# Optimization experiments

Hardware: AMD Instinct MI355X
Metric: run time of the kernel (lower is better)

The kernel has to match this reference:

```python
import jax, jax.numpy as jnp
import numpy as np
import math

DIM = 1024
NUM_HEADS = 16
QUANTUM_HEADS = 2
HEAD_DIM = DIM // NUM_HEADS          # 64
TRAD_HEADS = NUM_HEADS - QUANTUM_HEADS  # 14
B, S = 1, 1024
STEPS = 2048
LN_EPS = 1e-5


def setup_inputs() -> dict:
    key = jax.random.key(0)
    ks = jax.random.split(key, 10)
    hd2 = 2 * HEAD_DIM
    return {
        "x": jax.random.normal(ks[0], (B, S, DIM), jnp.float32),
        # to_quantum_state: Linear(head_dim -> 2*head_dim) + LayerNorm + Tanh (shared across quantum heads)
        "qs_W": jax.random.normal(ks[1], (hd2, HEAD_DIM), jnp.float32) / math.sqrt(HEAD_DIM),
        "qs_b": jnp.zeros((hd2,), jnp.float32),
        "ln_g": jnp.ones((hd2,), jnp.float32),
        "ln_b": jnp.zeros((hd2,), jnp.float32),
        # per-quantum-head scalars
        "q_freq": jax.random.normal(ks[2], (QUANTUM_HEADS,), jnp.float32) * 0.02,
        "q_shift": jax.random.normal(ks[3], (QUANTUM_HEADS,), jnp.float32) * 0.02,
        # traditional head projections (no bias)
        "Wq": jax.random.normal(ks[4], (TRAD_HEADS * HEAD_DIM, DIM), jnp.float32) / math.sqrt(DIM),
        "Wk": jax.random.normal(ks[5], (TRAD_HEADS * HEAD_DIM, DIM), jnp.float32) / math.sqrt(DIM),
        "Wv": jax.random.normal(ks[6], (TRAD_HEADS * HEAD_DIM, DIM), jnp.float32) / math.sqrt(DIM),
        # output projection (with bias)
        "Wo": jax.random.normal(ks[7], (DIM, DIM), jnp.float32) / math.sqrt(DIM),
        "bo": jnp.zeros((DIM,), jnp.float32),
    }


def _layernorm(h, g, b):
    mu = jnp.mean(h, axis=-1, keepdims=True)
    var = jnp.mean(jnp.square(h - mu), axis=-1, keepdims=True)
    return (h - mu) * jax.lax.rsqrt(var + LN_EPS) * g + b


def _forward(x, qs_W, qs_b, ln_g, ln_b, q_freq, q_shift, Wq, Wk, Wv, Wo, bo):
    cos_table = jnp.cos(jnp.linspace(0.0, 2.0 * math.pi, STEPS).astype(jnp.float32))
    scale = 1.0 / math.sqrt(HEAD_DIM)
    two_pi = 2.0 * math.pi

    outs = []
    # ---- quantum heads (small fixed loop over structurally distinct heads) ----
    for h in range(QUANTUM_HEADS):
        xh = x[..., h * HEAD_DIM:(h + 1) * HEAD_DIM]          # (B,S,hd)
        qs = jnp.tanh(_layernorm(xh @ qs_W.T + qs_b, ln_g, ln_b))  # (B,S,2hd)
        amp, phase = jnp.split(qs, 2, axis=-1)                 # each (B,S,hd)
        # per (query pos i, key pos j, feature d) phase difference
        pd = (phase[:, :, None, :] - phase[:, None, :, :]) * q_freq[h] + q_shift[h]  # (B,S,S,hd)
        idx = jnp.floor(jnp.mod(pd / two_pi * STEPS, STEPS)).astype(jnp.int32)
        interf = cos_table[idx]                                # lookup-table gather, (B,S,S,hd)
        attn = jnp.einsum('bid,bjd,bijd->bij', amp, amp, interf) * scale
        attn = jax.nn.softmax(attn, axis=-1)
        outs.append(attn @ xh)                                 # (B,S,hd), values are the raw head slice

    # ---- traditional heads: standard multi-head attention ----
    q = (x @ Wq.T).reshape(B, S, TRAD_HEADS, HEAD_DIM)
    k = (x @ Wk.T).reshape(B, S, TRAD_HEADS, HEAD_DIM)
    v = (x @ Wv.T).reshape(B, S, TRAD_HEADS, HEAD_DIM)
    scores = jnp.einsum('bqhd,bkhd->bhqk', q, k) * scale       # (B,Ht,S,S)
    probs = jax.nn.softmax(scores, axis=-1)
    trad = jnp.einsum('bhqk,bkhd->bqhd', probs, v).reshape(B, S, TRAD_HEADS * HEAD_DIM)
    outs.append(trad)

    out = jnp.concatenate(outs, axis=-1)                       # (B,S,DIM)
    return out @ Wo.T + bo


def reference(x, qs_W, qs_b, ln_g, ln_b, q_freq, q_shift, Wq, Wk, Wv, Wo, bo):
    return _forward(x, qs_W, qs_b, ln_g, ln_b, q_freq, q_shift, Wq, Wk, Wv, Wo, bo)
```

## Files before the change

kernel.cpp:

```cpp
#include <hip/hip_runtime.h>
#include <hip/hip_bf16.h>
#include <math.h>

#define DIMX 1024
#define SEQ  1024
#define HD   64
#define QH   2
#define TH   14
#define QKVN 2688
#define LN_EPS 1e-5f
#define NB_F2B 4736
#define NB_QPREP 1024
#define NB_XT 32

typedef __bf16 bf16x8 __attribute__((ext_vector_type(8)));
typedef float  f32x4  __attribute__((ext_vector_type(4)));
typedef unsigned short u16x8 __attribute__((ext_vector_type(8)));

__device__ inline unsigned short f2b_rne(float f) {
  unsigned int u = __float_as_uint(f);
  unsigned int r = (u + 0x7FFF + ((u >> 16) & 1)) >> 16;
  return (unsigned short)r;
}

__device__ inline float waveRedSum(float v) {
  #pragma unroll
  for (int off = 32; off; off >>= 1) v += __shfl_xor(v, off, 64);
  return v;
}

__global__ __launch_bounds__(256) void k_prep(
    const float* __restrict__ x, const float* __restrict__ qsW,
    const float* __restrict__ qsb, const float* __restrict__ lng,
    const float* __restrict__ lnb, const float* __restrict__ qfreq,
    const float* __restrict__ qshift,
    const float* __restrict__ wq, const float* __restrict__ wk,
    const float* __restrict__ wv, const float* __restrict__ wo,
    unsigned short* __restrict__ x_bf, unsigned short* __restrict__ wqkv_bf,
    unsigned short* __restrict__ wo_bf,
    unsigned short* __restrict__ qcs, unsigned short* __restrict__ kcs,
    unsigned short* __restrict__ xt) {
  __shared__ float xrow2[2][HD];
  __shared__ float redm[2][2], redv[2][2];
  __shared__ float qsv2[2][128];
  __shared__ unsigned short ttile[64][72];
  int t = threadIdx.x;
  int bid = blockIdx.x;
  if (bid < NB_F2B) {
    long i = ((long)bid * 256 + t) * 4;
    float4 v;
    unsigned short* dst;
    if (i < 1048576) {
      v = *reinterpret_cast<const float4*>(x + i);
      dst = x_bf + i;
    } else if (i < 3801088) {
      long j = i - 1048576;
      const float* s = (j < 917504) ? wq + j
                     : (j < 1835008) ? wk + (j - 917504)
                                     : wv + (j - 1835008);
      v = *reinterpret_cast<const float4*>(s);
      dst = wqkv_bf + j;
    } else {
      long j = i - 3801088;
      v = *reinterpret_cast<const float4*>(wo + j);
      dst = wo_bf + j;
    }
    ushort4 o;
    o.x = f2b_rne(v.x); o.y = f2b_rne(v.y); o.z = f2b_rne(v.z); o.w = f2b_rne(v.w);
    *reinterpret_cast<ushort4*>(dst) = o;
  } else if (bid < NB_F2B + NB_QPREP) {
    int half = t >> 7, o = t & 127;
    int row = (bid - NB_F2B) * 2 + half;
    int h = row >> 10, i = row & 1023;
    if (o < HD) xrow2[half][o] = x[i * DIMX + h * HD + o];
    __syncthreads();
    float s = qsb[o];
    #pragma unroll
    for (int d = 0; d < HD; d += 4) {
      float4 w = *reinterpret_cast<const float4*>(qsW + o * HD + d);
      float4 xv = *reinterpret_cast<const float4*>(&xrow2[half][d]);
      s += xv.x * w.x + xv.y * w.y + xv.z * w.z + xv.w * w.w;
    }
    int wid = (o >> 6), lane = o & 63;
    float ws = waveRedSum(s);
    if (lane == 0) redm[half][wid] = ws;
    __syncthreads();
    float mu = (redm[half][0] + redm[half][1]) * (1.0f / 128.0f);
    float dv = s - mu;
    float ws2 = waveRedSum(dv * dv);
    if (lane == 0) redv[half][wid] = ws2;
    __syncthreads();
    float var = (redv[half][0] + redv[half][1]) * (1.0f / 128.0f);
    float y = dv * rsqrtf(var + LN_EPS) * lng[o] + lnb[o];
    qsv2[half][o] = tanhf(y);
    __syncthreads();
    float freq = qfreq[h], shift = qshift[h];
    size_t base = ((size_t)h * 1024 + i) * 128;
    if (o < HD) {
      float amp = qsv2[half][o];
      float a = qsv2[half][64 + o] * freq + shift;
      float sn, cs;
      __sincosf(a, &sn, &cs);
      qcs[base + o]      = f2b_rne(amp * cs);
      qcs[base + 64 + o] = f2b_rne(amp * sn);
    } else {
      int d = o - 64;
      float amp = qsv2[half][d];
      float bAng = qsv2[half][64 + d] * freq;
      float sn, cs;
      __sincosf(bAng, &sn, &cs);
      kcs[base + d]      = f2b_rne(amp * cs);
      kcs[base + 64 + d] = f2b_rne(amp * sn);
    }
  } else {
    int b = bid - (NB_F2B + NB_QPREP);
    int h = b >> 4, kv0 = (b & 15) * 64;
    #pragma unroll
    for (int pass = 0; pass < 2; ++pass) {
      int s = pass * 256 + t;
      int r = s >> 3, c8 = (s & 7) * 8;
      const float* src = x + (size_t)(kv0 + r) * DIMX + h * 64 + c8;
      float4 a = *reinterpret_cast<const float4*>(src);
      float4 b4 = *reinterpret_cast<const float4*>(src + 4);
      ushort4 o1, o2;
      o1.x = f2b_rne(a.x);  o1.y = f2b_rne(a.y);  o1.z = f2b_rne(a.z);  o1.w = f2b_rne(a.w);
      o2.x = f2b_rne(b4.x); o2.y = f2b_rne(b4.y); o2.z = f2b_rne(b4.z); o2.w = f2b_rne(b4.w);
      *reinterpret_cast<ushort4*>(&ttile[r][c8]) = o1;
      *reinterpret_cast<ushort4*>(&ttile[r][c8 + 4]) = o2;
    }
    __syncthreads();
    #pragma unroll
    for (int pass = 0; pass < 2; ++pass) {
      int s = pass * 256 + t;
      int d = s >> 3, k8 = (s & 7) * 8;
      u16x8 o;
      #pragma unroll
      for (int j = 0; j < 8; ++j) o[j] = ttile[k8 + j][d];
      *reinterpret_cast<u16x8*>(xt + (size_t)h * 65536 + (size_t)d * 1024 + kv0 + k8) = o;
    }
  }
}

template <int DQK, int NT>
__device__ __forceinline__ void dev_fattn2(
    char* smem,
    const unsigned short* __restrict__ Qp, int ldq,
    const unsigned short* __restrict__ Kp, int ldk,
    const unsigned short* __restrict__ Vp,
    int q0, int kv0, int slot,
    float* __restrict__ pout, float* __restrict__ pml) {
  const int LQ = DQK + 8;
  const int KREG = DQK / 32;
  unsigned short* KV0 = (unsigned short*)smem;
  unsigned short* KV1 = KV0 + 64 * LQ;
  unsigned short* Ps  = KV1 + 64 * LQ;
  int t = threadIdx.x, lane = t & 63, w = t >> 6;
  int g = lane >> 4, li = lane & 15;

  bf16x8 aq[KREG];
  #pragma unroll
  for (int kk = 0; kk < KREG; ++kk)
    aq[kk] = *reinterpret_cast<const bf16x8*>(
        Qp + (size_t)(q0 + w * 16 + li) * ldq + kk * 32 + g * 8);

  u16x8 kreg[KREG], vreg[2];
  auto loadK = [&](int tile) {
    int j0 = kv0 + tile * 64;
    #pragma unroll
    for (int i = 0; i < KREG; ++i) {
      int s = i * 256 + t;
      int r = s / (DQK / 8), c8 = (s % (DQK / 8)) * 8;
      kreg[i] = *reinterpret_cast<const u16x8*>(Kp + (size_t)(j0 + r) * ldk + c8);
    }
  };
  auto writeK = [&](int buf) {
    unsigned short* Kd = buf ? KV1 : KV0;
    #pragma unroll
    for (int i = 0; i < KREG; ++i) {
      int s = i * 256 + t;
      int r = s / (DQK / 8), c8 = (s % (DQK / 8)) * 8;
      *reinterpret_cast<u16x8*>(&Kd[r * LQ + c8]) = kreg[i];
    }
  };
  auto loadV = [&](int tile) {
    int j0 = kv0 + tile * 64;
    #pragma unroll
    for (int i = 0; i < 2; ++i) {
      int s = i * 256 + t;
      int d = s >> 3, c8 = (s & 7) * 8;
      vreg[i] = *reinterpret_cast<const u16x8*>(Vp + (size_t)d * 1024 + j0 + c8);
    }
  };
  auto writeV = [&](int buf) {
    unsigned short* Vd = buf ? KV1 : KV0;
    #pragma unroll
    for (int i = 0; i < 2; ++i) {
      int s = i * 256 + t;
      int d = s >> 3, c8 = (s & 7) * 8;
      *reinterpret_cast<u16x8*>(&Vd[d * 72 + c8]) = vreg[i];
    }
  };

  loadK(0); writeK(0);
  if (NT > 1) loadK(1);
  loadV(0);
  __syncthreads();

  f32x4 s_all[NT][4] = {};

  #pragma unroll
  for (int tile = 0; tile < NT; ++tile) {
    const unsigned short* Ksc = (tile & 1) ? KV1 : KV0;
    if (tile < NT - 1) writeK((tile + 1) & 1);
    if (tile < NT - 2) loadK(tile + 2);
    if (tile == NT - 1) writeV(0);
    #pragma unroll
    for (int kk = 0; kk < KREG; ++kk) {
      #pragma unroll
      for (int n = 0; n < 4; ++n) {
        bf16x8 bk = *reinterpret_cast<const bf16x8*>(&Ksc[(n * 16 + li) * LQ + kk * 32 + g * 8]);
        s_all[tile][n] = __builtin_amdgcn_mfma_f32_16x16x32_bf16(aq[kk], bk, s_all[tile][n], 0, 0, 0);
      }
    }
    __syncthreads();
  }

  if (NT > 1) loadV(1);

  float mrow[4], lrow[4];
  #pragma unroll
  for (int r = 0; r < 4; ++r) {
    float tm = -1e30f;
    #pragma unroll
    for (int tile = 0; tile < NT; ++tile)
      #pragma unroll
      for (int n = 0; n < 4; ++n) tm = fmaxf(tm, s_all[tile][n][r]);
    #pragma unroll
    for (int m = 1; m < 16; m <<= 1) tm = fmaxf(tm, __shfl_xor(tm, m, 64));
    float rs = 0.f;
    #pragma unroll
    for (int tile = 0; tile < NT; ++tile)
      #pragma unroll
      for (int n = 0; n < 4; ++n) {
        float p = __expf((s_all[tile][n][r] - tm) * 0.125f);
        s_all[tile][n][r] = p;
        rs += p;
      }
    #pragma unroll
    for (int m = 1; m < 16; m <<= 1) rs += __shfl_xor(rs, m, 64);
    mrow[r] = tm; lrow[r] = rs;
  }

  f32x4 acc_o[4] = {};
  #pragma unroll
  for (int tile = 0; tile < NT; ++tile) {
    const unsigned short* Vsc = (tile & 1) ? KV1 : KV0;
    if (tile < NT - 1) writeV((tile + 1) & 1);
    if (tile < NT - 2) loadV(tile + 2);
    #pragma unroll
    for (int n = 0; n < 4; ++n)
      #pragma unroll
      for (int r = 0; r < 4; ++r)
        Ps[(w * 16 + g * 4 + r) * 72 + n * 16 + li] = f2b_rne(s_all[tile][n][r]);
    #pragma unroll
    for (int kk = 0; kk < 2; ++kk) {
      bf16x8 ap = *reinterpret_cast<const bf16x8*>(&Ps[(w * 16 + li) * 72 + kk * 32 + g * 8]);
      #pragma unroll
      for (int n = 0; n < 4; ++n) {
        bf16x8 bv = *reinterpret_cast<const bf16x8*>(&Vsc[(n * 16 + li) * 72 + kk * 32 + g * 8]);
        acc_o[n] = __builtin_amdgcn_mfma_f32_16x16x32_bf16(ap, bv, acc_o[n], 0, 0, 0);
      }
    }
    __syncthreads();
  }

  size_t rowbase = (size_t)slot * 1024;
  #pragma unroll
  for (int r = 0; r < 4; ++r) {
    int qr = q0 + w * 16 + g * 4 + r;
    #pragma unroll
    for (int n = 0; n < 4; ++n)
      pout[(rowbase + qr) * 64 + n * 16 + li] = acc_o[n][r];
    if (li == 0) {
      pml[(rowbase + qr) * 2 + 0] = mrow[r];
      pml[(rowbase + qr) * 2 + 1] = lrow[r];
    }
  }
}

template <int HAS_BIAS, int BF16_OUT>
__device__ __forceinline__ void dev_gemm64(
    char* smem,
    const unsigned short* __restrict__ A, const unsigned short* __restrict__ B,
    void* __restrict__ Cv, const float* __restrict__ bias,
    unsigned short* __restrict__ vtp,
    int bx, int by, int K, int lda, int ldb, int ldc) {
  unsigned short* As = (unsigned short*)smem;
  unsigned short* Bs = As + 64 * 128;
  int t = threadIdx.x, lane = t & 63, w = t >> 6;
  int wr = w >> 1, wc = w & 1;
  int g = lane >> 4, li = lane & 15;
  int mb = by * 64, nb = bx * 64;
  int rstg = t >> 4;
  int cs = t & 15;
  f32x4 acc[2][2] = {};
  for (int kb = 0; kb < K; kb += 128) {
    __syncthreads();
    #pragma unroll
    for (int i = 0; i < 4; ++i) {
      int row = i * 16 + rstg;
      int csw = ((cs ^ (row & 7)) * 8);
      __builtin_amdgcn_global_load_lds(
          (const __attribute__((address_space(1))) unsigned int*)(A + (size_t)(mb + row) * lda + kb + csw),
          (__attribute__((address_space(3))) unsigned int*)(As + row * 128 + cs * 8), 16, 0, 0);
      __builtin_amdgcn_global_load_lds(
          (const __attribute__((address_space(1))) unsigned int*)(B + (size_t)(nb + row) * ldb + kb + csw),
          (__attribute__((address_space(3))) unsigned int*)(Bs + row * 128 + cs * 8), 16, 0, 0);
    }
    __syncthreads();
    #pragma unroll
    for (int kk = 0; kk < 4; ++kk) {
      bf16x8 af[2], bfr[2];
      #pragma unroll
      for (int m = 0; m < 2; ++m) {
        int r = wr * 32 + m * 16 + li;
        int cb = kk * 4 + g;
        af[m] = *reinterpret_cast<const bf16x8*>(&As[r * 128 + ((cb ^ (r & 7)) * 8)]);
      }
      #pragma unroll
      for (int n = 0; n < 2; ++n) {
        int r = wc * 32 + n * 16 + li;
        int cb = kk * 4 + g;
        bfr[n] = *reinterpret_cast<const bf16x8*>(&Bs[r * 128 + ((cb ^ (r & 7)) * 8)]);
      }
      #pragma unroll
      for (int m = 0; m < 2; ++m)
        #pragma unroll
        for (int n = 0; n < 2; ++n)
          acc[m][n] = __builtin_amdgcn_mfma_f32_16x16x32_bf16(af[m], bfr[n], acc[m][n], 0, 0, 0);
    }
  }
  if (vtp != nullptr && nb >= 1792) {
    #pragma unroll
    for (int m = 0; m < 2; ++m) {
      int row0 = mb + wr * 32 + m * 16 + g * 4;
      #pragma unroll
      for (int n = 0; n < 2; ++n) {
        int colrel = nb - 1792 + wc * 32 + n * 16 + li;
        #pragma unroll
        for (int r = 0; r < 4; ++r)
          vtp[(size_t)colrel * 1024 + row0 + r] = f2b_rne(acc[m][n][r]);
      }
    }
    return;
  }
  #pragma unroll
  for (int m = 0; m < 2; ++m) {
    int row0 = mb + wr * 32 + m * 16 + g * 4;
    #pragma unroll
    for (int n = 0; n < 2; ++n) {
      int col = nb + wc * 32 + n * 16 + li;
      float bval = HAS_BIAS ? bias[col] : 0.0f;
      #pragma unroll
      for (int r = 0; r < 4; ++r) {
        size_t idx = (size_t)(row0 + r) * ldc + col;
        if (BF16_OUT) ((unsigned short*)Cv)[idx] = f2b_rne(acc[m][n][r] + bval);
        else          ((float*)Cv)[idx] = acc[m][n][r] + bval;
      }
    }
  }
}

__global__ __launch_bounds__(256) void k_qkvq(
    const unsigned short* __restrict__ x_bf, const unsigned short* __restrict__ wqkv,
    unsigned short* __restrict__ qkv, unsigned short* __restrict__ vt,
    const unsigned short* __restrict__ qcs, const unsigned short* __restrict__ kcs,
    const unsigned short* __restrict__ xt,
    float* __restrict__ pout, float* __restrict__ pml) {
  __shared__ __align__(16) char smem[44032];
  int bid = blockIdx.x;
  if (bid < 256) {
    int qt = bid & 15, h = (bid >> 4) & 1, split = bid >> 5;
    dev_fattn2<128, 2>(smem, qcs + (size_t)h * SEQ * 128, 128,
                       kcs + (size_t)h * SEQ * 128, 128,
                       xt + (size_t)h * 65536,
                       qt * 64, split * 128, h * 8 + split, pout, pml);
  } else {
    int gb = bid - 256;
    int swz = (gb & 7) * 84 + (gb >> 3);
    int by = swz / 42, bx = swz % 42;
    dev_gemm64<0, 1>(smem, x_bf, wqkv, qkv, nullptr, vt, bx, by, DIMX, DIMX, DIMX, QKVN);
  }
}

__global__ __launch_bounds__(256) void k_tattn(
    const unsigned short* __restrict__ qkv, const unsigned short* __restrict__ vt,
    float* __restrict__ pout, float* __restrict__ pml) {
  __shared__ __align__(16) char smem[27648];
  int bid = blockIdx.x;
  int swz = (bid & 7) * 112 + (bid >> 3);
  int qt = swz & 15, hs = swz >> 4;
  int h = hs % 14, split = hs / 14;
  dev_fattn2<64, 4>(smem, qkv + h * 64, QKVN,
                    qkv + 896 + h * 64, QKVN,
                    vt + (size_t)h * 65536,
                    qt * 64, split * 256, 16 + h * 4 + split, pout, pml);
}

__global__ __launch_bounds__(256) void k_fmerge(
    const float* __restrict__ pout, const float* __restrict__ pml,
    unsigned short* __restrict__ concat) {
  int rq = blockIdx.x * 4 + (threadIdx.x >> 6);
  int lh = rq >> 10, q = rq & 1023;
  int d = threadIdx.x & 63;
  int s0 = (lh < 2) ? lh * 8 : 16 + (lh - 2) * 4;
  int ns = (lh < 2) ? 8 : 4;
  float m_s[8], l_s[8];
  float M = -1e30f;
  #pragma unroll
  for (int s = 0; s < 8; ++s) {
    if (s < ns) {
      size_t rb = (size_t)(s0 + s) * 1024 + q;
      m_s[s] = pml[rb * 2 + 0];
      l_s[s] = pml[rb * 2 + 1];
      M = fmaxf(M, m_s[s]);
    }
  }
  float num = 0.f, den = 0.f;
  #pragma unroll
  for (int s = 0; s < 8; ++s) {
    if (s < ns) {
      float wgt = __expf((m_s[s] - M) * 0.125f);
      num += wgt * pout[((size_t)(s0 + s) * 1024 + q) * 64 + d];
      den += wgt * l_s[s];
    }
  }
  concat[(size_t)q * DIMX + lh * 64 + d] = f2b_rne(num / den);
}

__global__ __launch_bounds__(256) void k_oproj(
    const unsigned short* __restrict__ concat, const unsigned short* __restrict__ wo_bf,
    float* __restrict__ out, const float* __restrict__ bo) {
  __shared__ __align__(16) char smem[32768];
  int bid = blockIdx.x;
  int swz = (bid & 7) * 32 + (bid >> 3);
  int by = swz / 16, bx = swz % 16;
  dev_gemm64<1, 0>(smem, concat, wo_bf, out, bo, nullptr, bx, by, DIMX, DIMX, DIMX, DIMX);
}

extern "C" void kernel_launch(void* const* d_in, const int* in_sizes, int n_in,
                              void* d_out, int out_size, void* d_ws, size_t ws_size,
                              hipStream_t stream) {
  const float* x      = (const float*)d_in[0];
  const float* qsW    = (const float*)d_in[1];
  const float* qsb    = (const float*)d_in[2];
  const float* lng    = (const float*)d_in[3];
  const float* lnb    = (const float*)d_in[4];
  const float* qfreq  = (const float*)d_in[5];
  const float* qshift = (const float*)d_in[6];
  const float* Wq     = (const float*)d_in[7];
  const float* Wk     = (const float*)d_in[8];
  const float* Wv     = (const float*)d_in[9];
  const float* Wo     = (const float*)d_in[10];
  const float* bo     = (const float*)d_in[11];
  float* out = (float*)d_out;

  char* ws = (char*)d_ws;
  size_t off = 0;
  auto alloc = [&](size_t bytes) { char* p = ws + off; off += (bytes + 255) & ~(size_t)255; return p; };
  unsigned short* x_bf      = (unsigned short*)alloc((size_t)SEQ * DIMX * 2);
  unsigned short* wqkv_bf   = (unsigned short*)alloc((size_t)QKVN * DIMX * 2);
  unsigned short* wo_bf     = (unsigned short*)alloc((size_t)DIMX * DIMX * 2);
  unsigned short* concat_bf = (unsigned short*)alloc((size_t)SEQ * DIMX * 2);
  unsigned short* qkv_bf    = (unsigned short*)alloc((size_t)SEQ * QKVN * 2);
  unsigned short* qcs       = (unsigned short*)alloc((size_t)QH * SEQ * 128 * 2);
  unsigned short* kcs       = (unsigned short*)alloc((size_t)QH * SEQ * 128 * 2);
  unsigned short* vt        = (unsigned short*)alloc((size_t)TH * HD * SEQ * 2);
  unsigned short* xt        = (unsigned short*)alloc((size_t)QH * HD * SEQ * 2);
  float*          pout      = (float*)alloc((size_t)72 * SEQ * 64 * 4);
  float*          pml       = (float*)alloc((size_t)72 * SEQ * 2 * 4);

  k_prep<<<NB_F2B + NB_QPREP + NB_XT, 256, 0, stream>>>(
      x, qsW, qsb, lng, lnb, qfreq, qshift, Wq, Wk, Wv, Wo,
      x_bf, wqkv_bf, wo_bf, qcs, kcs, xt);

  k_qkvq<<<928, 256, 0, stream>>>(x_bf, wqkv_bf, qkv_bf, vt, qcs, kcs, xt, pout, pml);

  k_tattn<<<896, 256, 0, stream>>>(qkv_bf, vt, pout, pml);

  k_fmerge<<<16 * SEQ / 4, 256, 0, stream>>>(pout, pml, concat_bf);

  k_oproj<<<256, 256, 0, stream>>>(concat_bf, wo_bf, out, bo);
}
```

Baseline: 77.66 us.

## Fuse split-KV attention merge into per-block intra-warp KV split kernel

Replaces the split-KV flash attention (partial outputs to global plus a separate merge kernel) with a kernel where each block handles 16 query rows and its four warps split the KV range, merging through shared memory and writing bf16 concat directly. K and V are read straight from global memory instead of being staged through LDS. The quantum-head attention moves out of the QKV GEMM kernel into the unified attention launch. The output projection is retiled to 32x64 blocks for more blocks. This removes the pout/pml round trip and one launch, but drops LDS reuse of K/V across the block and serializes the quantum attention after the GEMM.

```diff
diff --git a/kernel.cpp b/kernel.cpp
--- a/kernel.cpp
+++ b/kernel.cpp
@@ -141,153 +141,6 @@
   }
 }
 
-template <int DQK, int NT>
-__device__ __forceinline__ void dev_fattn2(
-    char* smem,
-    const unsigned short* __restrict__ Qp, int ldq,
-    const unsigned short* __restrict__ Kp, int ldk,
-    const unsigned short* __restrict__ Vp,
-    int q0, int kv0, int slot,
-    float* __restrict__ pout, float* __restrict__ pml) {
-  const int LQ = DQK + 8;
-  const int KREG = DQK / 32;
-  unsigned short* KV0 = (unsigned short*)smem;
-  unsigned short* KV1 = KV0 + 64 * LQ;
-  unsigned short* Ps  = KV1 + 64 * LQ;
-  int t = threadIdx.x, lane = t & 63, w = t >> 6;
-  int g = lane >> 4, li = lane & 15;
-
-  bf16x8 aq[KREG];
-  #pragma unroll
-  for (int kk = 0; kk < KREG; ++kk)
-    aq[kk] = *reinterpret_cast<const bf16x8*>(
-        Qp + (size_t)(q0 + w * 16 + li) * ldq + kk * 32 + g * 8);
-
-  u16x8 kreg[KREG], vreg[2];
-  auto loadK = [&](int tile) {
-    int j0 = kv0 + tile * 64;
-    #pragma unroll
-    for (int i = 0; i < KREG; ++i) {
-      int s = i * 256 + t;
-      int r = s / (DQK / 8), c8 = (s % (DQK / 8)) * 8;
-      kreg[i] = *reinterpret_cast<const u16x8*>(Kp + (size_t)(j0 + r) * ldk + c8);
-    }
-  };
-  auto writeK = [&](int buf) {
-    unsigned short* Kd = buf ? KV1 : KV0;
-    #pragma unroll
-    for (int i = 0; i < KREG; ++i) {
-      int s = i * 256 + t;
-      int r = s / (DQK / 8), c8 = (s % (DQK / 8)) * 8;
-      *reinterpret_cast<u16x8*>(&Kd[r * LQ + c8]) = kreg[i];
-    }
-  };
-  auto loadV = [&](int tile) {
-    int j0 = kv0 + tile * 64;
-    #pragma unroll
-    for (int i = 0; i < 2; ++i) {
-      int s = i * 256 + t;
-      int d = s >> 3, c8 = (s & 7) * 8;
-      vreg[i] = *reinterpret_cast<const u16x8*>(Vp + (size_t)d * 1024 + j0 + c8);
-    }
-  };
-  auto writeV = [&](int buf) {
-    unsigned short* Vd = buf ? KV1 : KV0;
-    #pragma unroll
-    for (int i = 0; i < 2; ++i) {
-      int s = i * 256 + t;
-      int d = s >> 3, c8 = (s & 7) * 8;
-      *reinterpret_cast<u16x8*>(&Vd[d * 72 + c8]) = vreg[i];
-    }
-  };
-
-  loadK(0); writeK(0);
-  if (NT > 1) loadK(1);
-  loadV(0);
-  __syncthreads();
-
-  f32x4 s_all[NT][4] = {};
-
-  #pragma unroll
-  for (int tile = 0; tile < NT; ++tile) {
-    const unsigned short* Ksc = (tile & 1) ? KV1 : KV0;
-    if (tile < NT - 1) writeK((tile + 1) & 1);
-    if (tile < NT - 2) loadK(tile + 2);
-    if (tile == NT - 1) writeV(0);
-    #pragma unroll
-    for (int kk = 0; kk < KREG; ++kk) {
-      #pragma unroll
-      for (int n = 0; n < 4; ++n) {
-        bf16x8 bk = *reinterpret_cast<const bf16x8*>(&Ksc[(n * 16 + li) * LQ + kk * 32 + g * 8]);
-        s_all[tile][n] = __builtin_amdgcn_mfma_f32_16x16x32_bf16(aq[kk], bk, s_all[tile][n], 0, 0, 0);
-      }
-    }
-    __syncthreads();
-  }
-
-  if (NT > 1) loadV(1);
-
-  float mrow[4], lrow[4];
-  #pragma unroll
-  for (int r = 0; r < 4; ++r) {
-    float tm = -1e30f;
-    #pragma unroll
-    for (int tile = 0; tile < NT; ++tile)
-      #pragma unroll
-      for (int n = 0; n < 4; ++n) tm = fmaxf(tm, s_all[tile][n][r]);
-    #pragma unroll
-    for (int m = 1; m < 16; m <<= 1) tm = fmaxf(tm, __shfl_xor(tm, m, 64));
-    float rs = 0.f;
-    #pragma unroll
-    for (int tile = 0; tile < NT; ++tile)
-      #pragma unroll
-      for (int n = 0; n < 4; ++n) {
-        float p = __expf((s_all[tile][n][r] - tm) * 0.125f);
-        s_all[tile][n][r] = p;
-        rs += p;
-      }
-    #pragma unroll
-    for (int m = 1; m < 16; m <<= 1) rs += __shfl_xor(rs, m, 64);
-    mrow[r] = tm; lrow[r] = rs;
-  }
-
-  f32x4 acc_o[4] = {};
-  #pragma unroll
-  for (int tile = 0; tile < NT; ++tile) {
-    const unsigned short* Vsc = (tile & 1) ? KV1 : KV0;
-    if (tile < NT - 1) writeV((tile + 1) & 1);
-    if (tile < NT - 2) loadV(tile + 2);
-    #pragma unroll
-    for (int n = 0; n < 4; ++n)
-      #pragma unroll
-      for (int r = 0; r < 4; ++r)
-        Ps[(w * 16 + g * 4 + r) * 72 + n * 16 + li] = f2b_rne(s_all[tile][n][r]);
-    #pragma unroll
-    for (int kk = 0; kk < 2; ++kk) {
-      bf16x8 ap = *reinterpret_cast<const bf16x8*>(&Ps[(w * 16 + li) * 72 + kk * 32 + g * 8]);
-      #pragma unroll
-      for (int n = 0; n < 4; ++n) {
-        bf16x8 bv = *reinterpret_cast<const bf16x8*>(&Vsc[(n * 16 + li) * 72 + kk * 32 + g * 8]);
-        acc_o[n] = __builtin_amdgcn_mfma_f32_16x16x32_bf16(ap, bv, acc_o[n], 0, 0, 0);
-      }
-    }
-    __syncthreads();
-  }
-
-  size_t rowbase = (size_t)slot * 1024;
-  #pragma unroll
-  for (int r = 0; r < 4; ++r) {
-    int qr = q0 + w * 16 + g * 4 + r;
-    #pragma unroll
-    for (int n = 0; n < 4; ++n)
-      pout[(rowbase + qr) * 64 + n * 16 + li] = acc_o[n][r];
-    if (li == 0) {
-      pml[(rowbase + qr) * 2 + 0] = mrow[r];
-      pml[(rowbase + qr) * 2 + 1] = lrow[r];
-    }
-  }
-}
-
 template <int HAS_BIAS, int BF16_OUT>
 __device__ __forceinline__ void dev_gemm64(
     char* smem,
@@ -371,81 +224,207 @@
   }
 }
 
-__global__ __launch_bounds__(256) void k_qkvq(
+__global__ __launch_bounds__(256) void k_qkv(
     const unsigned short* __restrict__ x_bf, const unsigned short* __restrict__ wqkv,
-    unsigned short* __restrict__ qkv, unsigned short* __restrict__ vt,
-    const unsigned short* __restrict__ qcs, const unsigned short* __restrict__ kcs,
-    const unsigned short* __restrict__ xt,
-    float* __restrict__ pout, float* __restrict__ pml) {
-  __shared__ __align__(16) char smem[44032];
-  int bid = blockIdx.x;
-  if (bid < 256) {
-    int qt = bid & 15, h = (bid >> 4) & 1, split = bid >> 5;
-    dev_fattn2<128, 2>(smem, qcs + (size_t)h * SEQ * 128, 128,
-                       kcs + (size_t)h * SEQ * 128, 128,
-                       xt + (size_t)h * 65536,
-                       qt * 64, split * 128, h * 8 + split, pout, pml);
-  } else {
-    int gb = bid - 256;
-    int swz = (gb & 7) * 84 + (gb >> 3);
-    int by = swz / 42, bx = swz % 42;
-    dev_gemm64<0, 1>(smem, x_bf, wqkv, qkv, nullptr, vt, bx, by, DIMX, DIMX, DIMX, QKVN);
-  }
-}
-
-__global__ __launch_bounds__(256) void k_tattn(
-    const unsigned short* __restrict__ qkv, const unsigned short* __restrict__ vt,
-    float* __restrict__ pout, float* __restrict__ pml) {
-  __shared__ __align__(16) char smem[27648];
-  int bid = blockIdx.x;
-  int swz = (bid & 7) * 112 + (bid >> 3);
-  int qt = swz & 15, hs = swz >> 4;
-  int h = hs % 14, split = hs / 14;
-  dev_fattn2<64, 4>(smem, qkv + h * 64, QKVN,
-                    qkv + 896 + h * 64, QKVN,
-                    vt + (size_t)h * 65536,
-                    qt * 64, split * 256, 16 + h * 4 + split, pout, pml);
-}
-
-__global__ __launch_bounds__(256) void k_fmerge(
-    const float* __restrict__ pout, const float* __restrict__ pml,
-    unsigned short* __restrict__ concat) {
-  int rq = blockIdx.x * 4 + (threadIdx.x >> 6);
-  int lh = rq >> 10, q = rq & 1023;
-  int d = threadIdx.x & 63;
-  int s0 = (lh < 2) ? lh * 8 : 16 + (lh - 2) * 4;
-  int ns = (lh < 2) ? 8 : 4;
-  float m_s[8], l_s[8];
-  float M = -1e30f;
-  #pragma unroll
-  for (int s = 0; s < 8; ++s) {
-    if (s < ns) {
-      size_t rb = (size_t)(s0 + s) * 1024 + q;
-      m_s[s] = pml[rb * 2 + 0];
-      l_s[s] = pml[rb * 2 + 1];
-      M = fmaxf(M, m_s[s]);
-    }
-  }
-  float num = 0.f, den = 0.f;
-  #pragma unroll
-  for (int s = 0; s < 8; ++s) {
-    if (s < ns) {
-      float wgt = __expf((m_s[s] - M) * 0.125f);
-      num += wgt * pout[((size_t)(s0 + s) * 1024 + q) * 64 + d];
-      den += wgt * l_s[s];
-    }
-  }
-  concat[(size_t)q * DIMX + lh * 64 + d] = f2b_rne(num / den);
-}
-
-__global__ __launch_bounds__(256) void k_oproj(
-    const unsigned short* __restrict__ concat, const unsigned short* __restrict__ wo_bf,
-    float* __restrict__ out, const float* __restrict__ bo) {
+    unsigned short* __restrict__ qkv, unsigned short* __restrict__ vt) {
   __shared__ __align__(16) char smem[32768];
   int bid = blockIdx.x;
-  int swz = (bid & 7) * 32 + (bid >> 3);
-  int by = swz / 16, bx = swz % 16;
-  dev_gemm64<1, 0>(smem, concat, wo_bf, out, bo, nullptr, bx, by, DIMX, DIMX, DIMX, DIMX);
+  int swz = (bid & 7) * 84 + (bid >> 3);
+  int by = swz / 42, bx = swz % 42;
+  dev_gemm64<0, 1>(smem, x_bf, wqkv, qkv, nullptr, vt, bx, by, DIMX, DIMX, DIMX, QKVN);
+}
+
+template <int DQK>
+__device__ __forceinline__ void dev_fattn3(
+    const unsigned short* __restrict__ Qp, int ldq,
+    const unsigned short* __restrict__ Kp, int ldk,
+    const unsigned short* __restrict__ Vp,
+    int q0, int col0, unsigned short* __restrict__ concat) {
+  const int KREG = DQK / 32;
+  __shared__ float ml[4][16][2];
+  __shared__ float Op[4][16][68];
+  __shared__ unsigned short Ps[4][16 * 72];
+  int t = threadIdx.x, lane = t & 63, w = t >> 6;
+  int g = lane >> 4, li = lane & 15;
+
+  bf16x8 aq[KREG];
+  #pragma unroll
+  for (int kk = 0; kk < KREG; ++kk)
+    aq[kk] = *reinterpret_cast<const bf16x8*>(
+        Qp + (size_t)(q0 + li) * ldq + kk * 32 + g * 8);
+
+  int kvw = w * 256;
+  f32x4 s_all[4][4] = {};
+
+  #pragma unroll
+  for (int tau = 0; tau < 4; ++tau) {
+    int j0 = kvw + tau * 64;
+    #pragma unroll
+    for (int kk = 0; kk < KREG; ++kk) {
+      #pragma unroll
+      for (int n = 0; n < 4; ++n) {
+        bf16x8 bk = *reinterpret_cast<const bf16x8*>(
+            Kp + (size_t)(j0 + n * 16 + li) * ldk + kk * 32 + g * 8);
+        s_all[tau][n] = __builtin_amdgcn_mfma_f32_16x16x32_bf16(aq[kk], bk, s_all[tau][n], 0, 0, 0);
+      }
+    }
+  }
+
+  float mrow[4], lrow[4];
+  #pragma unroll
+  for (int r = 0; r < 4; ++r) {
+    float tm = -1e30f;
+    #pragma unroll
+    for (int tau = 0; tau < 4; ++tau)
+      #pragma unroll
+      for (int n = 0; n < 4; ++n) tm = fmaxf(tm, s_all[tau][n][r]);
+    #pragma unroll
+    for (int m = 1; m < 16; m <<= 1) tm = fmaxf(tm, __shfl_xor(tm, m, 64));
+    float rs = 0.f;
+    #pragma unroll
+    for (int tau = 0; tau < 4; ++tau)
+      #pragma unroll
+      for (int n = 0; n < 4; ++n) {
+        float p = __expf((s_all[tau][n][r] - tm) * 0.125f);
+        s_all[tau][n][r] = p;
+        rs += p;
+      }
+    #pragma unroll
+    for (int m = 1; m < 16; m <<= 1) rs += __shfl_xor(rs, m, 64);
+    mrow[r] = tm; lrow[r] = rs;
+  }
+  if (li == 0) {
+    #pragma unroll
+    for (int r = 0; r < 4; ++r) {
+      ml[w][g * 4 + r][0] = mrow[r];
+      ml[w][g * 4 + r][1] = lrow[r];
+    }
+  }
+  __syncthreads();
+  float fac[4];
+  #pragma unroll
+  for (int r = 0; r < 4; ++r) {
+    int row = g * 4 + r;
+    float M = fmaxf(fmaxf(ml[0][row][0], ml[1][row][0]),
+                    fmaxf(ml[2][row][0], ml[3][row][0]));
+    fac[r] = __expf((mrow[r] - M) * 0.125f);
+  }
+
+  f32x4 acc_o[4] = {};
+  #pragma unroll
+  for (int tau = 0; tau < 4; ++tau) {
+    int j0 = kvw + tau * 64;
+    #pragma unroll
+    for (int n = 0; n < 4; ++n)
+      #pragma unroll
+      for (int r = 0; r < 4; ++r)
+        Ps[w][(g * 4 + r) * 72 + n * 16 + li] = f2b_rne(s_all[tau][n][r] * fac[r]);
+    #pragma unroll
+    for (int kk = 0; kk < 2; ++kk) {
+      bf16x8 ap = *reinterpret_cast<const bf16x8*>(&Ps[w][li * 72 + kk * 32 + g * 8]);
+      #pragma unroll
+      for (int n = 0; n < 4; ++n) {
+        bf16x8 bv = *reinterpret_cast<const bf16x8*>(
+            Vp + (size_t)(n * 16 + li) * 1024 + j0 + kk * 32 + g * 8);
+        acc_o[n] = __builtin_amdgcn_mfma_f32_16x16x32_bf16(ap, bv, acc_o[n], 0, 0, 0);
+      }
+    }
+  }
+  #pragma unroll
+  for (int n = 0; n < 4; ++n)
+    #pragma unroll
+    for (int r = 0; r < 4; ++r)
+      Op[w][g * 4 + r][n * 16 + li] = acc_o[n][r];
+  __syncthreads();
+
+  #pragma unroll
+  for (int e = t; e < 1024; e += 256) {
+    int row = e >> 6, d = e & 63;
+    float M = fmaxf(fmaxf(ml[0][row][0], ml[1][row][0]),
+                    fmaxf(ml[2][row][0], ml[3][row][0]));
+    float L = 0.f, O = 0.f;
+    #pragma unroll
+    for (int w2 = 0; w2 < 4; ++w2) {
+      L += ml[w2][row][1] * __expf((ml[w2][row][0] - M) * 0.125f);
+      O += Op[w2][row][d];
+    }
+    concat[(size_t)(q0 + row) * DIMX + col0 + d] = f2b_rne(O / L);
+  }
+}
+
+__global__ __launch_bounds__(256) void k_attn(
+    const unsigned short* __restrict__ qkv, const unsigned short* __restrict__ vt,
+    const unsigned short* __restrict__ qcs, const unsigned short* __restrict__ kcs,
+    const unsigned short* __restrict__ xt, unsigned short* __restrict__ concat) {
+  int bid = blockIdx.x;
+  int l = (bid & 7) * 128 + (bid >> 3);
+  if (l < 896) {
+    int h = l >> 6, qt = l & 63;
+    dev_fattn3<64>(qkv + h * 64, QKVN, qkv + 896 + h * 64, QKVN,
+                   vt + (size_t)h * 65536, qt * 16, 128 + h * 64, concat);
+  } else {
+    int b2 = l - 896;
+    int h = b2 >> 6, qt = b2 & 63;
+    dev_fattn3<128>(qcs + (size_t)h * SEQ * 128, 128, kcs + (size_t)h * SEQ * 128, 128,
+                    xt + (size_t)h * 65536, qt * 16, h * 64, concat);
+  }
+}
+
+__global__ __launch_bounds__(256) void k_oproj(
+    const unsigned short* __restrict__ A, const unsigned short* __restrict__ B,
+    float* __restrict__ C, const float* __restrict__ bias) {
+  __shared__ unsigned short As[32 * 128];
+  __shared__ unsigned short Bs[64 * 128];
+  int bid = blockIdx.x;
+  int swz = (bid & 7) * 64 + (bid >> 3);
+  int by = swz >> 4, bx = swz & 15;
+  int t = threadIdx.x, lane = t & 63, w = t >> 6;
+  int wr = w & 1, wc = w >> 1;
+  int g = lane >> 4, li = lane & 15;
+  int mb = by * 32, nb = bx * 64;
+  int rstg = t >> 4, cs = t & 15;
+  f32x4 acc[2] = {};
+  for (int kb = 0; kb < DIMX; kb += 128) {
+    __syncthreads();
+    #pragma unroll
+    for (int i = 0; i < 2; ++i) {
+      int row = i * 16 + rstg;
+      int csw = ((cs ^ (row & 7)) * 8);
+      __builtin_amdgcn_global_load_lds(
+          (const __attribute__((address_space(1))) unsigned int*)(A + (size_t)(mb + row) * DIMX + kb + csw),
+          (__attribute__((address_space(3))) unsigned int*)(As + row * 128 + cs * 8), 16, 0, 0);
+    }
+    #pragma unroll
+    for (int i = 0; i < 4; ++i) {
+      int row = i * 16 + rstg;
+      int csw = ((cs ^ (row & 7)) * 8);
+      __builtin_amdgcn_global_load_lds(
+          (const __attribute__((address_space(1))) unsigned int*)(B + (size_t)(nb + row) * DIMX + kb + csw),
+          (__attribute__((address_space(3))) unsigned int*)(Bs + row * 128 + cs * 8), 16, 0, 0);
+    }
+    __syncthreads();
+    #pragma unroll
+    for (int kk = 0; kk < 4; ++kk) {
+      int cb = kk * 4 + g;
+      int ra = wr * 16 + li;
+      bf16x8 af = *reinterpret_cast<const bf16x8*>(&As[ra * 128 + ((cb ^ (ra & 7)) * 8)]);
+      #pragma unroll
+      for (int n = 0; n < 2; ++n) {
+        int rb = wc * 32 + n * 16 + li;
+        bf16x8 bfr = *reinterpret_cast<const bf16x8*>(&Bs[rb * 128 + ((cb ^ (rb & 7)) * 8)]);
+        acc[n] = __builtin_amdgcn_mfma_f32_16x16x32_bf16(af, bfr, acc[n], 0, 0, 0);
+      }
+    }
+  }
+  int row0 = mb + wr * 16 + g * 4;
+  #pragma unroll
+  for (int n = 0; n < 2; ++n) {
+    int col = nb + wc * 32 + n * 16 + li;
+    float bval = bias[col];
+    #pragma unroll
+    for (int r = 0; r < 4; ++r)
+      C[(size_t)(row0 + r) * DIMX + col] = acc[n][r] + bval;
+  }
 }
 
 extern "C" void kernel_launch(void* const* d_in, const int* in_sizes, int n_in,
@@ -477,18 +456,14 @@
   unsigned short* kcs       = (unsigned short*)alloc((size_t)QH * SEQ * 128 * 2);
   unsigned short* vt        = (unsigned short*)alloc((size_t)TH * HD * SEQ * 2);
   unsigned short* xt        = (unsigned short*)alloc((size_t)QH * HD * SEQ * 2);
-  float*          pout      = (float*)alloc((size_t)72 * SEQ * 64 * 4);
-  float*          pml       = (float*)alloc((size_t)72 * SEQ * 2 * 4);
 
   k_prep<<<NB_F2B + NB_QPREP + NB_XT, 256, 0, stream>>>(
       x, qsW, qsb, lng, lnb, qfreq, qshift, Wq, Wk, Wv, Wo,
       x_bf, wqkv_bf, wo_bf, qcs, kcs, xt);
 
-  k_qkvq<<<928, 256, 0, stream>>>(x_bf, wqkv_bf, qkv_bf, vt, qcs, kcs, xt, pout, pml);
-
-  k_tattn<<<896, 256, 0, stream>>>(qkv_bf, vt, pout, pml);
-
-  k_fmerge<<<16 * SEQ / 4, 256, 0, stream>>>(pout, pml, concat_bf);
-
-  k_oproj<<<256, 256, 0, stream>>>(concat_bf, wo_bf, out, bo);
-}
+  k_qkv<<<672, 256, 0, stream>>>(x_bf, wqkv_bf, qkv_bf, vt);
+
+  k_attn<<<1024, 256, 0, stream>>>(qkv_bf, vt, qcs, kcs, xt, concat_bf);
+
+  k_oproj<<<512, 256, 0, stream>>>(concat_bf, wo_bf, out, bo);
+}
```

Result: slower. 96.88 us (+24.7%).
